# Kernel tuning notes

Measured on AMD Instinct MI355X. Metric: run time of the kernel, lower is better.

## Reference

```python
import jax, jax.numpy as jnp
import numpy as np

B, T, C = 2, 2048, 1024
H, HD = 16, 64
M = 256  # per memory bank
K_CANON = 4


def setup_inputs() -> dict:
    key = jax.random.key(0)
    ks = jax.random.split(key, 10)
    s = 0.02
    return {
        "x": jax.random.normal(ks[0], (B, T, C), jnp.float32),
        "fwd_mem": jax.random.normal(ks[1], (B, M, C), jnp.float32),
        "rev_mem": jax.random.normal(ks[2], (B, M, C), jnp.float32),
        "Wq": jax.random.normal(ks[3], (C, C), jnp.float32) * s,
        "Wk": jax.random.normal(ks[4], (C, C), jnp.float32) * s,
        "Wv": jax.random.normal(ks[5], (C, C), jnp.float32) * s,
        "Wo": jax.random.normal(ks[6], (C, C), jnp.float32) * s,
        "gate_w": jax.random.normal(ks[7], (H, C), jnp.float32) * s,
        "gate_b": jnp.zeros((H,), jnp.float32),
        "canon_w": jax.random.normal(ks[8], (C, 1, K_CANON), jnp.float32) * s,
        "canon_bias": jax.random.normal(ks[9], (C,), jnp.float32) * s,
    }


def _canon_conv(y, canon_w, canon_bias):
    # causal depthwise conv1d with residual; torch weight [C,1,K] -> WIO kernel [K,1,C]
    kern = jnp.transpose(canon_w, (2, 1, 0))
    y_pad = jnp.pad(y, ((0, 0), (K_CANON - 1, 0), (0, 0)))
    conv = jax.lax.conv_general_dilated(
        y_pad, kern, window_strides=(1,), padding='VALID',
        dimension_numbers=('NWC', 'WIO', 'NWC'), feature_group_count=C)
    return y + conv + canon_bias


def reference(x, fwd_mem, rev_mem, Wq, Wk, Wv, Wo, gate_w, gate_b, canon_w, canon_bias):
    Bn, Tn, Cn = x.shape
    scale = 1.0 / np.sqrt(HD)

    q = x @ Wq.T  # [B,T,C]
    k = x @ Wk.T
    v = x @ Wv.T
    # memory integration: project memories with same k/v proj, concat on seq dim
    k = jnp.concatenate([k, fwd_mem @ Wk.T, rev_mem @ Wk.T], axis=1)  # [B,S,C]
    v = jnp.concatenate([v, fwd_mem @ Wv.T, rev_mem @ Wv.T], axis=1)
    S = k.shape[1]
    mem_len = S - Tn

    def heads(t):
        return t.reshape(Bn, -1, H, HD).transpose(0, 2, 1, 3)  # [B,h,S,hd]

    qh, kh, vh = heads(q), heads(k), heads(v)
    scores = jnp.einsum('bhtd,bhsd->bhts', qh, kh) * scale  # [B,h,T,S]
    # causal mask over the first T key columns; memory columns fully visible
    causal = jnp.triu(jnp.ones((Tn, Tn), bool), k=1)
    full_mask = jnp.pad(causal, ((0, 0), (0, mem_len)))  # [T,S]
    scores = jnp.where(full_mask[None, None], -jnp.inf, scores)
    w = jax.nn.softmax(scores, axis=-1)

    # split chunk vs memory, gate memory contribution per head
    w_chunk, w_mem = w[..., :Tn], w[..., Tn:]
    v_chunk, v_mem = vh[:, :, :Tn], vh[:, :, Tn:]
    Y_chunk = jnp.einsum('bhts,bhsd->bhtd', w_chunk, v_chunk)
    Y_mem = jnp.einsum('bhtm,bhmd->bhtd', w_mem, v_mem)
    g = jax.nn.sigmoid(q @ gate_w.T + gate_b)  # [B,T,h]
    g = g.transpose(0, 2, 1)[..., None]  # [B,h,T,1]
    Y = Y_chunk + g * Y_mem

    attn_out = Y.transpose(0, 2, 1, 3).reshape(Bn, Tn, Cn)
    attn_out = _canon_conv(attn_out, canon_w, canon_bias)
    return attn_out @ Wo.T
```

## Files before the change

### kernel.cpp

```cpp
#include <hip/hip_runtime.h>
#include <hip/hip_bf16.h>
#include <cstdint>


typedef __bf16 bf16x8_t __attribute__((ext_vector_type(8)));
typedef __bf16 bf16x4_t __attribute__((ext_vector_type(4)));
typedef float f32x4_t __attribute__((ext_vector_type(4)));

__device__ __forceinline__ f32x4_t mfma16(bf16x8_t a, bf16x8_t b, f32x4_t c) {
    return __builtin_amdgcn_mfma_f32_16x16x32_bf16(a, b, c, 0, 0, 0);
}

__device__ __forceinline__ void gl2lds16(const void* g, void* l) {
    __builtin_amdgcn_global_load_lds(
        (__attribute__((address_space(1))) uint32_t*)(uintptr_t)g,
        (__attribute__((address_space(3))) uint32_t*)l, 16, 0, 0);
}

#define OFF_X   0
#define OFF_FWD 4194304
#define OFF_REV 4718592
#define OFF_WQ  5242880
#define OFF_WK  6291456
#define OFF_WV  7340032
#define OFF_WO  8388608
#define OFF_GW  9437184
#define OFF_GB  9453568
#define OFF_CW  9453584
#define OFF_CB  9457680
#define N_TOT   9458704

__global__ __launch_bounds__(256) void conv_all_kernel(
    const void* p0, const void* p1, const void* p2, const void* p3,
    const void* p4, const void* p5, const void* p6, const void* p7,
    const void* p8, const void* p9, const void* p10,
    __hip_bfloat16* __restrict__ arena)
{
    const int i = (blockIdx.x * 256 + threadIdx.x) * 4;
    if (i >= N_TOT) return;
    const void* src; int off;
    if      (i < OFF_FWD) { src = p0;  off = OFF_X;   }
    else if (i < OFF_REV) { src = p1;  off = OFF_FWD; }
    else if (i < OFF_WQ)  { src = p2;  off = OFF_REV; }
    else if (i < OFF_WK)  { src = p3;  off = OFF_WQ;  }
    else if (i < OFF_WV)  { src = p4;  off = OFF_WK;  }
    else if (i < OFF_WO)  { src = p5;  off = OFF_WV;  }
    else if (i < OFF_GW)  { src = p6;  off = OFF_WO;  }
    else if (i < OFF_GB)  { src = p7;  off = OFF_GW;  }
    else if (i < OFF_CW)  { src = p8;  off = OFF_GB;  }
    else if (i < OFF_CB)  { src = p9;  off = OFF_CW;  }
    else                  { src = p10; off = OFF_CB;  }
    const int j = i - off;
    const float4 f = *(const float4*)((const float*)src + j);
    arena[i + 0] = __float2bfloat16(f.x);
    arena[i + 1] = __float2bfloat16(f.y);
    arena[i + 2] = __float2bfloat16(f.z);
    arena[i + 3] = __float2bfloat16(f.w);
}

__global__ __launch_bounds__(256) void gemm_bt_kernel(
    const __hip_bfloat16* __restrict__ A, const __hip_bfloat16* __restrict__ B,
    void* __restrict__ C, int ldc, int f32o)
{
    __shared__ __align__(16) __hip_bfloat16 As[128 * 32];
    __shared__ __align__(16) __hip_bfloat16 Bs[128 * 32];
    const int tid  = threadIdx.x;
    const int lane = tid & 63;
    const int wid  = tid >> 6;
    const int q4   = lane >> 4;
    const int c16  = lane & 15;
    const int wm   = (wid >> 1) * 64;
    const int wn   = (wid & 1) * 64;
    const size_t arow0 = (size_t)blockIdx.x * 128;
    const size_t brow0 = (size_t)blockIdx.y * 128;
    const int c0 = tid;
    const int c1 = tid + 256;
    const __hip_bfloat16* gA0 = A + (arow0 + (c0 >> 2)) * 1024 + ((c0 & 3) << 3);
    const __hip_bfloat16* gA1 = A + (arow0 + (c1 >> 2)) * 1024 + ((c1 & 3) << 3);
    const __hip_bfloat16* gB0 = B + (brow0 + (c0 >> 2)) * 1024 + ((c0 & 3) << 3);
    const __hip_bfloat16* gB1 = B + (brow0 + (c1 >> 2)) * 1024 + ((c1 & 3) << 3);

    f32x4_t acc[4][4];
#pragma unroll
    for (int i = 0; i < 4; ++i)
#pragma unroll
        for (int j = 0; j < 4; ++j)
#pragma unroll
            for (int r = 0; r < 4; ++r) acc[i][j][r] = 0.0f;

    for (int k0 = 0; k0 < 1024; k0 += 32) {
        gl2lds16(gA0 + k0, &As[c0 * 8]);
        gl2lds16(gA1 + k0, &As[c1 * 8]);
        gl2lds16(gB0 + k0, &Bs[c0 * 8]);
        gl2lds16(gB1 + k0, &Bs[c1 * 8]);
        __syncthreads();
        bf16x8_t af[4], bfr[4];
#pragma unroll
        for (int i = 0; i < 4; ++i)
            af[i] = *(const bf16x8_t*)&As[(wm + i * 16 + c16) * 32 + q4 * 8];
#pragma unroll
        for (int j = 0; j < 4; ++j)
            bfr[j] = *(const bf16x8_t*)&Bs[(wn + j * 16 + c16) * 32 + q4 * 8];
#pragma unroll
        for (int i = 0; i < 4; ++i)
#pragma unroll
            for (int j = 0; j < 4; ++j)
                acc[i][j] = mfma16(af[i], bfr[j], acc[i][j]);
        __syncthreads();
    }
#pragma unroll
    for (int i = 0; i < 4; ++i) {
        const int mg = (int)arow0 + wm + i * 16 + q4 * 4;
#pragma unroll
        for (int j = 0; j < 4; ++j) {
            const int ng = (int)brow0 + wn + j * 16 + c16;
#pragma unroll
            for (int r = 0; r < 4; ++r) {
                const size_t idx = (size_t)(mg + r) * ldc + ng;
                if (f32o) ((float*)C)[idx] = acc[i][j][r];
                else ((__hip_bfloat16*)C)[idx] = __float2bfloat16(acc[i][j][r]);
            }
        }
    }
}

__global__ __launch_bounds__(64) void gate_kernel(
    const __hip_bfloat16* __restrict__ Q, const __hip_bfloat16* __restrict__ gw,
    const __hip_bfloat16* __restrict__ gb, float* __restrict__ G)
{
    const int base = blockIdx.x * 16;
    const int lane = threadIdx.x;
    const int q4   = lane >> 4;
    const int c16  = lane & 15;
    f32x4_t acc = {0.0f, 0.0f, 0.0f, 0.0f};
    const __hip_bfloat16* qrow = Q + (size_t)(base + c16) * 1024 + q4 * 8;
    const __hip_bfloat16* wrow = gw + (size_t)c16 * 1024 + q4 * 8;
#pragma unroll
    for (int kk = 0; kk < 32; ++kk) {
        const bf16x8_t a = *(const bf16x8_t*)(qrow + kk * 32);
        const bf16x8_t w = *(const bf16x8_t*)(wrow + kk * 32);
        acc = mfma16(a, w, acc);
    }
    const float bias = __bfloat162float(gb[c16]);
#pragma unroll
    for (int r = 0; r < 4; ++r) {
        const int row = base + q4 * 4 + r;
        G[(size_t)row * 16 + c16] = 1.0f / (1.0f + __expf(-(acc[r] + bias)));
    }
}

#define PSTR 72
__global__ __launch_bounds__(256) void attn_kernel(
    const __hip_bfloat16* __restrict__ Q, const __hip_bfloat16* __restrict__ K,
    const __hip_bfloat16* __restrict__ Vt,
    const float* __restrict__ G, __hip_bfloat16* __restrict__ Y)
{
    __shared__ __align__(16) __hip_bfloat16 Ks[64 * 64];
    __shared__ __align__(16) __hip_bfloat16 Vs[64 * 64];
    __shared__ __align__(16) __hip_bfloat16 Plds[4][16 * PSTR];
    const int flat = blockIdx.x;
    const int bh   = flat & 31;
    const int tIdx = 31 - (flat >> 5);
    const int b    = bh >> 4;
    const int h    = bh & 15;
    const int tid  = threadIdx.x;
    const int wid  = tid >> 6;
    const int lane = tid & 63;
    const int q4   = lane >> 4;
    const int c16  = lane & 15;
    const int rowbase = tIdx * 64 + wid * 16;

    const __hip_bfloat16* qrow = Q + (size_t)(b * 2048 + rowbase + c16) * 1024 + h * 64;
    const bf16x8_t qa0 = *(const bf16x8_t*)(qrow + q4 * 8);
    const bf16x8_t qa1 = *(const bf16x8_t*)(qrow + 32 + q4 * 8);

    float rs[4], gate[4];
    f32x4_t acc[4];
#pragma unroll
    for (int fp = 0; fp < 4; ++fp)
#pragma unroll
        for (int r = 0; r < 4; ++r) acc[fp][r] = 0.0f;
#pragma unroll
    for (int r = 0; r < 4; ++r) {
        rs[r] = 0.0f;
        gate[r] = G[(size_t)(b * 2048 + rowbase + q4 * 4 + r) * 16 + h];
    }

    const int nCausal = tIdx + 1;
    const int nTiles  = nCausal + 8;
    auto kvRow = [&](int tile) -> int {
        if (tile < nCausal) return b * 2048 + tile * 64;
        const int mi = (tile - nCausal) * 64;
        return (mi < 256) ? 4096 + b * 256 + mi : 4608 + b * 256 + (mi - 256);
    };

    const int srow0 = tid >> 3,        sch0 = (tid & 7) ^ (srow0 & 7);
    const int srow1 = (tid + 256) >> 3, sch1 = (tid & 7) ^ (srow1 & 7);
    const int sw0 = (q4 ^ (c16 & 7)) * 8;
    const int sw1 = ((q4 + 4) ^ (c16 & 7)) * 8;

    for (int tile = 0; tile < nTiles; ++tile) {
        const bool isMem  = (tile >= nCausal);
        const bool isDiag = (tile == nCausal - 1);
        const int  vr     = kvRow(tile);
        __syncthreads();
        gl2lds16(K + (size_t)(vr + srow0) * 1024 + h * 64 + sch0 * 8, &Ks[tid * 8]);
        gl2lds16(K + (size_t)(vr + srow1) * 1024 + h * 64 + sch1 * 8, &Ks[(tid + 256) * 8]);
        gl2lds16(Vt + (size_t)(h * 64 + srow0) * 5120 + vr + sch0 * 8, &Vs[tid * 8]);
        gl2lds16(Vt + (size_t)(h * 64 + srow1) * 5120 + vr + sch1 * 8, &Vs[(tid + 256) * 8]);
        __syncthreads();
        bf16x8_t kb0[4], kb1[4], vb0[4], vb1[4];
#pragma unroll
        for (int f = 0; f < 4; ++f) {
            kb0[f] = *(const bf16x8_t*)&Ks[(f * 16 + c16) * 64 + sw0];
            kb1[f] = *(const bf16x8_t*)&Ks[(f * 16 + c16) * 64 + sw1];
            vb0[f] = *(const bf16x8_t*)&Vs[(f * 16 + c16) * 64 + sw0];
            vb1[f] = *(const bf16x8_t*)&Vs[(f * 16 + c16) * 64 + sw1];
        }
        f32x4_t sc[4];
#pragma unroll
        for (int f = 0; f < 4; ++f) {
            f32x4_t z = {0.0f, 0.0f, 0.0f, 0.0f};
            z = mfma16(qa0, kb0[f], z);
            z = mfma16(qa1, kb1[f], z);
            sc[f] = z;
        }
#pragma unroll
        for (int f = 0; f < 4; ++f)
#pragma unroll
            for (int r = 0; r < 4; ++r) {
                float p = __expf(sc[f][r] * 0.125f);
                if (isDiag) {
                    const int sg = tile * 64 + f * 16 + c16;
                    if (sg > rowbase + q4 * 4 + r) p = 0.0f;
                }
                rs[r] += p;
                if (isMem) p *= gate[r];
                Plds[wid][(q4 * 4 + r) * PSTR + f * 16 + c16] = __float2bfloat16(p);
            }
        const bf16x8_t pa0 = *(const bf16x8_t*)&Plds[wid][c16 * PSTR + q4 * 8];
        const bf16x8_t pa1 = *(const bf16x8_t*)&Plds[wid][c16 * PSTR + 32 + q4 * 8];
#pragma unroll
        for (int fp = 0; fp < 4; ++fp) {
            acc[fp] = mfma16(pa0, vb0[fp], acc[fp]);
            acc[fp] = mfma16(pa1, vb1[fp], acc[fp]);
        }
    }
#pragma unroll
    for (int m = 1; m <= 8; m <<= 1)
#pragma unroll
        for (int r = 0; r < 4; ++r) rs[r] += __shfl_xor(rs[r], m, 64);
    float inv[4];
#pragma unroll
    for (int r = 0; r < 4; ++r) inv[r] = 1.0f / rs[r];
#pragma unroll
    for (int fp = 0; fp < 4; ++fp)
#pragma unroll
        for (int r = 0; r < 4; ++r) {
            const int tg = rowbase + q4 * 4 + r;
            Y[(size_t)(b * 2048 + tg) * 1024 + h * 64 + fp * 16 + c16] =
                __float2bfloat16(acc[fp][r] * inv[r]);
        }
}

__global__ __launch_bounds__(256) void canon_kernel(
    const __hip_bfloat16* __restrict__ Yin, const __hip_bfloat16* __restrict__ cw,
    const __hip_bfloat16* __restrict__ cb, __hip_bfloat16* __restrict__ Yout)
{
    const int idx = (blockIdx.x * 256 + threadIdx.x) * 4;
    const int c = idx & 1023;
    const int t = (idx >> 10) & 2047;
    const bf16x4_t y0 = *(const bf16x4_t*)(Yin + idx);
    const bf16x4_t bb = *(const bf16x4_t*)(cb + c);
    float a[4];
#pragma unroll
    for (int i = 0; i < 4; ++i) a[i] = (float)y0[i] + (float)bb[i];
    const bf16x8_t w01 = *(const bf16x8_t*)(cw + c * 4);
    const bf16x8_t w23 = *(const bf16x8_t*)(cw + c * 4 + 8);
#pragma unroll
    for (int j = 0; j < 4; ++j) {
        if (t - 3 + j >= 0) {
            const bf16x4_t yj = *(const bf16x4_t*)(Yin + idx + (j - 3) * 1024);
            a[0] += (float)yj[0] * (float)w01[j];
            a[1] += (float)yj[1] * (float)w01[4 + j];
            a[2] += (float)yj[2] * (float)w23[j];
            a[3] += (float)yj[3] * (float)w23[4 + j];
        }
    }
    bf16x4_t o;
#pragma unroll
    for (int i = 0; i < 4; ++i) o[i] = (__bf16)a[i];
    *(bf16x4_t*)(Yout + idx) = o;
}

extern "C" void kernel_launch(void* const* d_in, const int* in_sizes, int n_in,
                              void* d_out, int out_size, void* d_ws, size_t ws_size,
                              hipStream_t stream)
{
    char* ws = (char*)d_ws;
    const size_t MB = 1ull << 20;
    if (ws_size < 57 * MB) return;

    __hip_bfloat16* arena = (__hip_bfloat16*)ws;
    __hip_bfloat16* Qb    = (__hip_bfloat16*)(ws + 20 * MB);
    __hip_bfloat16* Kall  = (__hip_bfloat16*)(ws + 28 * MB);
    __hip_bfloat16* Vt    = (__hip_bfloat16*)(ws + 38 * MB);
    float*          G     = (float*)(ws + 48 * MB);
    __hip_bfloat16* Y1    = (__hip_bfloat16*)(ws + 49 * MB);
    __hip_bfloat16* Y2    = Kall;

    const dim3 blk(256);
    conv_all_kernel<<<dim3((N_TOT / 4 + 255) / 256), blk, 0, stream>>>(
        d_in[0], d_in[1], d_in[2], d_in[3], d_in[4], d_in[5], d_in[6],
        d_in[7], d_in[8], d_in[9], d_in[10], arena);

    const __hip_bfloat16* xB  = arena + OFF_X;
    const __hip_bfloat16* WqB = arena + OFF_WQ;
    const __hip_bfloat16* WkB = arena + OFF_WK;
    const __hip_bfloat16* WvB = arena + OFF_WV;
    const __hip_bfloat16* WoB = arena + OFF_WO;

    gemm_bt_kernel<<<dim3(32, 8), blk, 0, stream>>>(xB,  WqB, Qb,   1024, 0);
    gemm_bt_kernel<<<dim3(40, 8), blk, 0, stream>>>(xB,  WkB, Kall, 1024, 0);
    gemm_bt_kernel<<<dim3(8, 40), blk, 0, stream>>>(WvB, xB,  Vt,   5120, 0);
    gate_kernel<<<dim3(256), dim3(64), 0, stream>>>(Qb, arena + OFF_GW, arena + OFF_GB, G);
    attn_kernel<<<dim3(1024), blk, 0, stream>>>(Qb, Kall, Vt, G, Y1);
    canon_kernel<<<dim3(4096), blk, 0, stream>>>(Y1, arena + OFF_CW, arena + OFF_CB, Y2);
    gemm_bt_kernel<<<dim3(32, 8), blk, 0, stream>>>(Y2, WoB, d_out, 1024, 1);
}
```

Measured before the change: 273.7 us.

## Fuse Q and K projections into one GEMM and shrink GEMM tile to 64x128

The separate Q and K projection GEMMs are merged into one launch that writes an interleaved QK buffer with row stride 2048. This relies on Wq and Wk being adjacent in the arena so they form one 2048-row weight. The GEMM kernel moves from 128x128 tiles with 4 waves to 64x128 tiles with 2 waves, which doubles the block count so the CUs fill better. The trade-off is less operand reuse per tile. The attention and gate kernels are updated for the new stride, and the workspace is repacked so Y1 overwrites the arena.

```diff
diff --git a/kernel.cpp b/kernel.cpp
--- a/kernel.cpp
+++ b/kernel.cpp
@@ -58,27 +58,27 @@
     arena[i + 3] = __float2bfloat16(f.w);
 }
 
-__global__ __launch_bounds__(256) void gemm_bt_kernel(
+__global__ __launch_bounds__(128) void gemm_bt_kernel(
     const __hip_bfloat16* __restrict__ A, const __hip_bfloat16* __restrict__ B,
     void* __restrict__ C, int ldc, int f32o)
 {
-    __shared__ __align__(16) __hip_bfloat16 As[128 * 32];
+    __shared__ __align__(16) __hip_bfloat16 As[64 * 32];
     __shared__ __align__(16) __hip_bfloat16 Bs[128 * 32];
     const int tid  = threadIdx.x;
     const int lane = tid & 63;
     const int wid  = tid >> 6;
     const int q4   = lane >> 4;
     const int c16  = lane & 15;
-    const int wm   = (wid >> 1) * 64;
-    const int wn   = (wid & 1) * 64;
-    const size_t arow0 = (size_t)blockIdx.x * 128;
+    const int wn   = wid * 64;
+    const size_t arow0 = (size_t)blockIdx.x * 64;
     const size_t brow0 = (size_t)blockIdx.y * 128;
-    const int c0 = tid;
-    const int c1 = tid + 256;
-    const __hip_bfloat16* gA0 = A + (arow0 + (c0 >> 2)) * 1024 + ((c0 & 3) << 3);
-    const __hip_bfloat16* gA1 = A + (arow0 + (c1 >> 2)) * 1024 + ((c1 & 3) << 3);
-    const __hip_bfloat16* gB0 = B + (brow0 + (c0 >> 2)) * 1024 + ((c0 & 3) << 3);
-    const __hip_bfloat16* gB1 = B + (brow0 + (c1 >> 2)) * 1024 + ((c1 & 3) << 3);
+    const int a0 = tid, a1 = tid + 128;
+    const __hip_bfloat16* gA0 = A + (arow0 + (a0 >> 2)) * 1024 + ((a0 & 3) << 3);
+    const __hip_bfloat16* gA1 = A + (arow0 + (a1 >> 2)) * 1024 + ((a1 & 3) << 3);
+    const __hip_bfloat16* gB0 = B + (brow0 + (a0 >> 2)) * 1024 + ((a0 & 3) << 3);
+    const __hip_bfloat16* gB1 = B + (brow0 + (a1 >> 2)) * 1024 + ((a1 & 3) << 3);
+    const __hip_bfloat16* gB2 = B + (brow0 + ((a0 + 256) >> 2)) * 1024 + ((a0 & 3) << 3);
+    const __hip_bfloat16* gB3 = B + (brow0 + ((a1 + 256) >> 2)) * 1024 + ((a1 & 3) << 3);
 
     f32x4_t acc[4][4];
 #pragma unroll
@@ -89,15 +89,17 @@
             for (int r = 0; r < 4; ++r) acc[i][j][r] = 0.0f;
 
     for (int k0 = 0; k0 < 1024; k0 += 32) {
-        gl2lds16(gA0 + k0, &As[c0 * 8]);
-        gl2lds16(gA1 + k0, &As[c1 * 8]);
-        gl2lds16(gB0 + k0, &Bs[c0 * 8]);
-        gl2lds16(gB1 + k0, &Bs[c1 * 8]);
+        gl2lds16(gA0 + k0, &As[a0 * 8]);
+        gl2lds16(gA1 + k0, &As[a1 * 8]);
+        gl2lds16(gB0 + k0, &Bs[a0 * 8]);
+        gl2lds16(gB1 + k0, &Bs[a1 * 8]);
+        gl2lds16(gB2 + k0, &Bs[(a0 + 256) * 8]);
+        gl2lds16(gB3 + k0, &Bs[(a1 + 256) * 8]);
         __syncthreads();
         bf16x8_t af[4], bfr[4];
 #pragma unroll
         for (int i = 0; i < 4; ++i)
-            af[i] = *(const bf16x8_t*)&As[(wm + i * 16 + c16) * 32 + q4 * 8];
+            af[i] = *(const bf16x8_t*)&As[(i * 16 + c16) * 32 + q4 * 8];
 #pragma unroll
         for (int j = 0; j < 4; ++j)
             bfr[j] = *(const bf16x8_t*)&Bs[(wn + j * 16 + c16) * 32 + q4 * 8];
@@ -110,7 +112,7 @@
     }
 #pragma unroll
     for (int i = 0; i < 4; ++i) {
-        const int mg = (int)arow0 + wm + i * 16 + q4 * 4;
+        const int mg = (int)arow0 + i * 16 + q4 * 4;
 #pragma unroll
         for (int j = 0; j < 4; ++j) {
             const int ng = (int)brow0 + wn + j * 16 + c16;
@@ -125,7 +127,7 @@
 }
 
 __global__ __launch_bounds__(64) void gate_kernel(
-    const __hip_bfloat16* __restrict__ Q, const __hip_bfloat16* __restrict__ gw,
+    const __hip_bfloat16* __restrict__ QK, const __hip_bfloat16* __restrict__ gw,
     const __hip_bfloat16* __restrict__ gb, float* __restrict__ G)
 {
     const int base = blockIdx.x * 16;
@@ -133,7 +135,7 @@
     const int q4   = lane >> 4;
     const int c16  = lane & 15;
     f32x4_t acc = {0.0f, 0.0f, 0.0f, 0.0f};
-    const __hip_bfloat16* qrow = Q + (size_t)(base + c16) * 1024 + q4 * 8;
+    const __hip_bfloat16* qrow = QK + (size_t)(base + c16) * 2048 + q4 * 8;
     const __hip_bfloat16* wrow = gw + (size_t)c16 * 1024 + q4 * 8;
 #pragma unroll
     for (int kk = 0; kk < 32; ++kk) {
@@ -151,7 +153,7 @@
 
 #define PSTR 72
 __global__ __launch_bounds__(256) void attn_kernel(
-    const __hip_bfloat16* __restrict__ Q, const __hip_bfloat16* __restrict__ K,
+    const __hip_bfloat16* __restrict__ QK,
     const __hip_bfloat16* __restrict__ Vt,
     const float* __restrict__ G, __hip_bfloat16* __restrict__ Y)
 {
@@ -170,7 +172,7 @@
     const int c16  = lane & 15;
     const int rowbase = tIdx * 64 + wid * 16;
 
-    const __hip_bfloat16* qrow = Q + (size_t)(b * 2048 + rowbase + c16) * 1024 + h * 64;
+    const __hip_bfloat16* qrow = QK + (size_t)(b * 2048 + rowbase + c16) * 2048 + h * 64;
     const bf16x8_t qa0 = *(const bf16x8_t*)(qrow + q4 * 8);
     const bf16x8_t qa1 = *(const bf16x8_t*)(qrow + 32 + q4 * 8);
 
@@ -194,18 +196,19 @@
         return (mi < 256) ? 4096 + b * 256 + mi : 4608 + b * 256 + (mi - 256);
     };
 
-    const int srow0 = tid >> 3,        sch0 = (tid & 7) ^ (srow0 & 7);
+    const int srow0 = tid >> 3,         sch0 = (tid & 7) ^ (srow0 & 7);
     const int srow1 = (tid + 256) >> 3, sch1 = (tid & 7) ^ (srow1 & 7);
     const int sw0 = (q4 ^ (c16 & 7)) * 8;
     const int sw1 = ((q4 + 4) ^ (c16 & 7)) * 8;
+    const __hip_bfloat16* Kbase = QK + 1024 + h * 64;
 
     for (int tile = 0; tile < nTiles; ++tile) {
         const bool isMem  = (tile >= nCausal);
         const bool isDiag = (tile == nCausal - 1);
         const int  vr     = kvRow(tile);
         __syncthreads();
-        gl2lds16(K + (size_t)(vr + srow0) * 1024 + h * 64 + sch0 * 8, &Ks[tid * 8]);
-        gl2lds16(K + (size_t)(vr + srow1) * 1024 + h * 64 + sch1 * 8, &Ks[(tid + 256) * 8]);
+        gl2lds16(Kbase + (size_t)(vr + srow0) * 2048 + sch0 * 8, &Ks[tid * 8]);
+        gl2lds16(Kbase + (size_t)(vr + srow1) * 2048 + sch1 * 8, &Ks[(tid + 256) * 8]);
         gl2lds16(Vt + (size_t)(h * 64 + srow0) * 5120 + vr + sch0 * 8, &Vs[tid * 8]);
         gl2lds16(Vt + (size_t)(h * 64 + srow1) * 5120 + vr + sch1 * 8, &Vs[(tid + 256) * 8]);
         __syncthreads();
@@ -299,15 +302,14 @@
 {
     char* ws = (char*)d_ws;
     const size_t MB = 1ull << 20;
-    if (ws_size < 57 * MB) return;
+    if (ws_size < 50 * MB) return;
 
     __hip_bfloat16* arena = (__hip_bfloat16*)ws;
-    __hip_bfloat16* Qb    = (__hip_bfloat16*)(ws + 20 * MB);
-    __hip_bfloat16* Kall  = (__hip_bfloat16*)(ws + 28 * MB);
-    __hip_bfloat16* Vt    = (__hip_bfloat16*)(ws + 38 * MB);
-    float*          G     = (float*)(ws + 48 * MB);
-    __hip_bfloat16* Y1    = (__hip_bfloat16*)(ws + 49 * MB);
-    __hip_bfloat16* Y2    = Kall;
+    __hip_bfloat16* QK    = (__hip_bfloat16*)(ws + 19 * MB);
+    __hip_bfloat16* Vt    = (__hip_bfloat16*)(ws + 39 * MB);
+    float*          G     = (float*)(ws + 49 * MB);
+    __hip_bfloat16* Y1    = (__hip_bfloat16*)ws;
+    __hip_bfloat16* Y2    = QK;
 
     const dim3 blk(256);
     conv_all_kernel<<<dim3((N_TOT / 4 + 255) / 256), blk, 0, stream>>>(
@@ -316,15 +318,13 @@
 
     const __hip_bfloat16* xB  = arena + OFF_X;
     const __hip_bfloat16* WqB = arena + OFF_WQ;
-    const __hip_bfloat16* WkB = arena + OFF_WK;
     const __hip_bfloat16* WvB = arena + OFF_WV;
     const __hip_bfloat16* WoB = arena + OFF_WO;
 
-    gemm_bt_kernel<<<dim3(32, 8), blk, 0, stream>>>(xB,  WqB, Qb,   1024, 0);
-    gemm_bt_kernel<<<dim3(40, 8), blk, 0, stream>>>(xB,  WkB, Kall, 1024, 0);
-    gemm_bt_kernel<<<dim3(8, 40), blk, 0, stream>>>(WvB, xB,  Vt,   5120, 0);
-    gate_kernel<<<dim3(256), dim3(64), 0, stream>>>(Qb, arena + OFF_GW, arena + OFF_GB, G);
-    attn_kernel<<<dim3(1024), blk, 0, stream>>>(Qb, Kall, Vt, G, Y1);
+    gemm_bt_kernel<<<dim3(80, 16), dim3(128), 0, stream>>>(xB,  WqB, QK, 2048, 0);
+    gemm_bt_kernel<<<dim3(16, 40), dim3(128), 0, stream>>>(WvB, xB,  Vt, 5120, 0);
+    gate_kernel<<<dim3(256), dim3(64), 0, stream>>>(QK, arena + OFF_GW, arena + OFF_GB, G);
+    attn_kernel<<<dim3(1024), blk, 0, stream>>>(QK, Vt, G, Y1);
     canon_kernel<<<dim3(4096), blk, 0, stream>>>(Y1, arena + OFF_CW, arena + OFF_CB, Y2);
-    gemm_bt_kernel<<<dim3(32, 8), blk, 0, stream>>>(Y2, WoB, d_out, 1024, 1);
-}
+    gemm_bt_kernel<<<dim3(64, 8), dim3(128), 0, stream>>>(Y2, WoB, d_out, 1024, 1);
+}
```

After: 269.3 us. About the same (-1.6%).
